# Kernel optimization log

Measured on AMD Instinct MI355X. Metric: run time of the kernel, lower is better.

Reference implementation:

```python
import jax, jax.numpy as jnp
import numpy as np

NUM_HEADS = 16


def setup_inputs() -> dict:
    key = jax.random.key(0)
    ks = jax.random.split(key, 4)
    B, S, H = 2, 2048, 1024
    hidden_states = jax.random.normal(ks[0], (B, S, H), dtype=jnp.float32)
    attention_mask = jnp.zeros((B, 1, 1, S), dtype=jnp.float32)
    scale = 1.0 / np.sqrt(H)
    Wq = jax.random.normal(ks[1], (H, H), dtype=jnp.float32) * scale
    Wk = jax.random.normal(ks[2], (H, H), dtype=jnp.float32) * scale
    Wv = jax.random.normal(ks[3], (H, H), dtype=jnp.float32) * scale
    bq = jnp.zeros((H,), dtype=jnp.float32)
    bk = jnp.zeros((H,), dtype=jnp.float32)
    bv = jnp.zeros((H,), dtype=jnp.float32)
    return {"hidden_states": hidden_states, "attention_mask": attention_mask,
            "Wq": Wq, "bq": bq, "Wk": Wk, "bk": bk, "Wv": Wv, "bv": bv}


def _split_heads(x, B, S):
    # [B, S, H] -> [B, h, S, d]
    return x.reshape(B, S, NUM_HEADS, -1).transpose(0, 2, 1, 3)


def reference(hidden_states, attention_mask, Wq, bq, Wk, bk, Wv, bv):
    B, S, H = hidden_states.shape
    d = H // NUM_HEADS
    q = _split_heads(hidden_states @ Wq + bq, B, S)  # [B,h,S,d]
    k = _split_heads(hidden_states @ Wk + bk, B, S)
    v = _split_heads(hidden_states @ Wv + bv, B, S)

    scores = jnp.einsum('bhqd,bhkd->bhqk', q, k) / jnp.sqrt(jnp.float32(d))
    # causal mask: -inf strictly above diagonal, plus additive pad mask
    i = jnp.arange(S)[:, None]
    j = jnp.arange(S)[None, :]
    causal = jnp.where(j > i, -jnp.inf, 0.0).astype(scores.dtype)  # [S,S]
    scores = scores + attention_mask + causal[None, None, :, :]

    probs = jax.nn.softmax(scores, axis=-1)  # dropout prob = 0.0 -> identity
    context = jnp.einsum('bhqk,bhkd->bhqd', probs, v)  # [B,h,S,d]
    return context.transpose(0, 2, 1, 3).reshape(B, S, H)
```

## Files before the change

kernel.cpp:

```cpp
#include <hip/hip_runtime.h>

typedef __attribute__((ext_vector_type(4)))  float f32x4;
typedef __attribute__((ext_vector_type(16))) float f32x16;
typedef __attribute__((ext_vector_type(8)))  short bf16x8;

typedef __attribute__((address_space(1))) const void gvoid;
typedef __attribute__((address_space(3))) void lvoid;

__device__ __forceinline__ void gl_lds16(const void* g, void* l) {
  __builtin_amdgcn_global_load_lds((gvoid*)g, (lvoid*)l, 16, 0, 0);
}

__device__ __forceinline__ ushort f2bf(float f) {
  union { float f; unsigned u; } v; v.f = f;
  unsigned u = v.u;
  return (ushort)((u + 0x7fffu + ((u >> 16) & 1u)) >> 16);
}

__device__ __forceinline__ uint cvt_pk_bf16(float lo, float hi) {
  uint r;
  asm("v_cvt_pk_bf16_f32 %0, %1, %2" : "=v"(r) : "v"(lo), "v"(hi));
  return r;
}
__device__ __forceinline__ void plswap(uint& x, uint& y) {
  asm volatile("v_permlane32_swap_b32 %0, %1" : "+v"(x), "+v"(y));
}

__global__ __launch_bounds__(256) void cvt_x(const float* __restrict__ x,
                                             ushort* __restrict__ o) {
  int idx = blockIdx.x * 256 + threadIdx.x;
  float4 v = reinterpret_cast<const float4*>(x)[idx];
  ushort4 r;
  r.x = f2bf(v.x); r.y = f2bf(v.y); r.z = f2bf(v.z); r.w = f2bf(v.w);
  reinterpret_cast<ushort4*>(o)[idx] = r;
}

__global__ __launch_bounds__(256) void wtrans(const float* __restrict__ Wq,
                                              const float* __restrict__ Wk,
                                              const float* __restrict__ Wv,
                                              ushort* __restrict__ WT) {
  __shared__ ushort tile[64 * 65];
  int bx = blockIdx.x;
  int w = bx >> 8;
  int rem = bx & 255;
  int k0 = (rem >> 4) << 6;
  int n0 = (rem & 15) << 6;
  const float* W = (w == 0) ? Wq : (w == 1) ? Wk : Wv;
  int tid = threadIdx.x;
#pragma unroll
  for (int it = 0; it < 16; ++it) {
    int idx = tid + it * 256;
    int r = idx >> 6, c = idx & 63;
    tile[r * 65 + c] = f2bf(W[(k0 + r) * 1024 + n0 + c]);
  }
  __syncthreads();
#pragma unroll
  for (int it = 0; it < 16; ++it) {
    int idx = tid + it * 256;
    int r = idx >> 6, c = idx & 63;
    WT[w * 1048576 + (n0 + r) * 1024 + k0 + c] = tile[c * 65 + r];
  }
}

__global__ __launch_bounds__(256) void qkv_gemm(
    const ushort* __restrict__ Xb, const ushort* __restrict__ WT,
    const float* __restrict__ bq, const float* __restrict__ bk,
    const float* __restrict__ bv, ushort* __restrict__ Qb,
    ushort* __restrict__ Kb, ushort* __restrict__ VT) {
  __shared__ ushort smem[128 * 136];
  ushort* Xs = smem;
  ushort* Ws = smem + 8192;
  int tid = threadIdx.x;
  int wave = tid >> 6, lane = tid & 63, g = lane >> 4, lr = lane & 15;
  int wr = wave >> 1, wc = wave & 1;
  int m0 = blockIdx.x << 7;
  int n0g = blockIdx.y << 7;
  f32x4 acc[4][4];
#pragma unroll
  for (int i = 0; i < 4; ++i)
#pragma unroll
    for (int j = 0; j < 4; ++j) { acc[i][j][0] = 0.f; acc[i][j][1] = 0.f; acc[i][j][2] = 0.f; acc[i][j][3] = 0.f; }

  int lrow = lane >> 3, lcol = (lane & 7) * 8;
  for (int k0 = 0; k0 < 1024; k0 += 64) {
    __syncthreads();
#pragma unroll
    for (int c = 0; c < 4; ++c) {
      int cw = wave * 4 + c;
      int row = cw * 8 + lrow;
      gl_lds16(Xb + (size_t)(m0 + row) * 1024 + k0 + lcol, Xs + cw * 512);
      gl_lds16(WT + (size_t)(n0g + row) * 1024 + k0 + lcol, Ws + cw * 512);
    }
    __syncthreads();
#pragma unroll
    for (int ks = 0; ks < 2; ++ks) {
      bf16x8 a[4], b[4];
#pragma unroll
      for (int mi = 0; mi < 4; ++mi)
        a[mi] = *reinterpret_cast<const bf16x8*>(&Xs[(wr * 64 + mi * 16 + lr) * 64 + ks * 32 + g * 8]);
#pragma unroll
      for (int ni = 0; ni < 4; ++ni)
        b[ni] = *reinterpret_cast<const bf16x8*>(&Ws[(wc * 64 + ni * 16 + lr) * 64 + ks * 32 + g * 8]);
      __builtin_amdgcn_s_setprio(1);
#pragma unroll
      for (int mi = 0; mi < 4; ++mi)
#pragma unroll
        for (int ni = 0; ni < 4; ++ni)
          acc[mi][ni] = __builtin_amdgcn_mfma_f32_16x16x32_bf16(a[mi], b[ni], acc[mi][ni], 0, 0, 0);
      __builtin_amdgcn_s_setprio(0);
    }
  }
  __syncthreads();

  int which = n0g >> 10;
  const float* bias = (which == 0) ? bq : (which == 1) ? bk : bv;
  int nloc0 = (n0g & 1023);
  if (which == 2) {
#pragma unroll
    for (int ni = 0; ni < 4; ++ni) {
      int row = wc * 64 + ni * 16 + lr;
      float bb = bias[nloc0 + row];
#pragma unroll
      for (int mi = 0; mi < 4; ++mi) {
        int m = wr * 64 + mi * 16 + g * 4;
        ushort4 v4;
        v4.x = f2bf(acc[mi][ni][0] + bb);
        v4.y = f2bf(acc[mi][ni][1] + bb);
        v4.z = f2bf(acc[mi][ni][2] + bb);
        v4.w = f2bf(acc[mi][ni][3] + bb);
        *reinterpret_cast<ushort4*>(&smem[row * 136 + m]) = v4;
      }
    }
    __syncthreads();
    int b_ = m0 >> 11, s0 = m0 & 2047;
#pragma unroll
    for (int it = 0; it < 8; ++it) {
      int c = tid + it * 256;
      int row = c >> 4, mc = (c & 15) * 8;
      uint4 vv = *reinterpret_cast<const uint4*>(&smem[row * 136 + mc]);
      int n = nloc0 + row;
      int hh = n >> 6, dd = n & 63;
      *reinterpret_cast<uint4*>(&VT[((size_t)(b_ * 16 + hh) * 64 + dd) * 2048 + s0 + mc]) = vv;
    }
  } else {
#pragma unroll
    for (int ni = 0; ni < 4; ++ni) {
      int n = wc * 64 + ni * 16 + lr;
      float bb = bias[nloc0 + n];
#pragma unroll
      for (int mi = 0; mi < 4; ++mi) {
#pragma unroll
        for (int r = 0; r < 4; ++r)
          smem[(wr * 64 + mi * 16 + g * 4 + r) * 136 + n] = f2bf(acc[mi][ni][r] + bb);
      }
    }
    __syncthreads();
    ushort* ob = (which == 0) ? Qb : Kb;
#pragma unroll
    for (int it = 0; it < 8; ++it) {
      int c = tid + it * 256;
      int row = c >> 4, nc = (c & 15) * 8;
      uint4 vv = *reinterpret_cast<const uint4*>(&smem[row * 136 + nc]);
      int m = m0 + row;
      int b_ = m >> 11, s = m & 2047;
      int n = nloc0 + nc;
      int hh = n >> 6, dd = n & 63;
      *reinterpret_cast<uint4*>(&ob[((size_t)(b_ * 16 + hh) * 2048 + s) * 64 + dd]) = vv;
    }
  }
}

__global__ __launch_bounds__(256) void attn(const ushort* __restrict__ Qb,
                                            const ushort* __restrict__ Kb,
                                            const ushort* __restrict__ VT,
                                            const float* __restrict__ mask,
                                            float* __restrict__ out) {
  __shared__ char smem[34816];
  ushort* Ks = (ushort*)smem;
  ushort* Vs = (ushort*)(smem + 8192);
  float*  Ms = (float*)(smem + 16384);
  int tid = threadIdx.x;
  int wave = tid >> 6, lane = tid & 63;
  int hi = lane >> 5, l31 = lane & 31;
  int pi = blockIdx.x & 15, bh = blockIdx.x >> 4;
  int b_ = bh >> 4, h = bh & 15;
  const ushort* Qh = Qb + (size_t)bh * 2048 * 64;
  const ushort* Kh = Kb + (size_t)bh * 2048 * 64;
  const ushort* VTh = VT + (size_t)bh * 64 * 2048;

  int tile = (wave < 2) ? pi : (31 - pi);
  int q0w = tile * 64 + (wave & 1) * 32;
  int tmax = 31 - pi;

  bf16x8 aq[4];
#pragma unroll
  for (int ds = 0; ds < 4; ++ds)
    aq[ds] = *reinterpret_cast<const bf16x8*>(Qh + (q0w + l31) * 64 + ds * 16 + hi * 8);

  f32x16 Od0, Od1;
#pragma unroll
  for (int j = 0; j < 16; ++j) { Od0[j] = 0.f; Od1[j] = 0.f; }
  float mrun = -__builtin_inff(), lrun = 0.f;

  for (int t = 0; t <= tmax; ++t) {
    int kv0 = t << 6;
    __syncthreads();
#pragma unroll
    for (int c = 0; c < 2; ++c) {
      int ch = tid + (c << 8);
      int row = ch >> 3, e0 = (ch & 7) * 8, bc = (ch & 7) << 4;
      int sw = bc ^ ((row & 7) << 4);
      uint4 kvv = *reinterpret_cast<const uint4*>(Kh + (size_t)(kv0 + row) * 64 + e0);
      *reinterpret_cast<uint4*>((char*)Ks + row * 128 + sw) = kvv;
      uint4 vvv = *reinterpret_cast<const uint4*>(VTh + (size_t)row * 2048 + kv0 + e0);
      *reinterpret_cast<uint4*>((char*)Vs + row * 128 + sw) = vvv;
    }
    if (tid < 64) Ms[tid] = mask[b_ * 2048 + kv0 + tid];
    __syncthreads();

#pragma unroll
    for (int sub = 0; sub < 2; ++sub) {
      int kvb = kv0 + sub * 32;
      if (kvb > q0w) continue;
      bool dg = (kvb == q0w);

      f32x16 s;
#pragma unroll
      for (int j = 0; j < 16; ++j) s[j] = 0.f;
      __builtin_amdgcn_s_setprio(1);
#pragma unroll
      for (int ds = 0; ds < 4; ++ds) {
        int krow = sub * 32 + l31;
        bf16x8 kf = *reinterpret_cast<const bf16x8*>(
            (char*)Ks + krow * 128 + ((ds * 32 + hi * 16) ^ ((krow & 7) << 4)));
        s = __builtin_amdgcn_mfma_f32_32x32x16_bf16(kf, aq[ds], s, 0, 0, 0);
      }
      __builtin_amdgcn_s_setprio(0);

#pragma unroll
      for (int jj = 0; jj < 4; ++jj) {
        float4 mv4 = *reinterpret_cast<const float4*>(Ms + sub * 32 + jj * 8 + 4 * hi);
        const float* mvp = (const float*)&mv4;
#pragma unroll
        for (int r = 0; r < 4; ++r) {
          int j = jj * 4 + r;
          float sv = s[j] * 0.125f + mvp[r];
          if (dg) {
            int kvg = kvb + jj * 8 + 4 * hi + r;
            sv = (kvg > q0w + l31) ? -__builtin_inff() : sv;
          }
          s[j] = sv;
        }
      }

      float tmx = s[0];
#pragma unroll
      for (int j = 1; j < 16; ++j) tmx = fmaxf(tmx, s[j]);
      tmx = fmaxf(tmx, __shfl_xor(tmx, 32));
      bool defer = __all(tmx - mrun <= 8.0f);
      float al = 1.0f;
      if (!defer) {
        float nm = fmaxf(mrun, tmx);
        al = __expf(mrun - nm);
        mrun = nm;
      }
      float rs = 0.f;
#pragma unroll
      for (int j = 0; j < 16; ++j) {
        float p = __expf(s[j] - mrun);
        s[j] = p;
        rs += p;
      }
      rs += __shfl_xor(rs, 32);
      lrun = lrun * al + rs;
      if (!defer) {
#pragma unroll
        for (int j = 0; j < 16; ++j) { Od0[j] *= al; Od1[j] *= al; }
      }

      uint x0 = cvt_pk_bf16(s[0], s[1]),   y0 = cvt_pk_bf16(s[4], s[5]);
      uint x1 = cvt_pk_bf16(s[2], s[3]),   y1 = cvt_pk_bf16(s[6], s[7]);
      plswap(x0, y0); plswap(x1, y1);
      uint x2 = cvt_pk_bf16(s[8], s[9]),   y2 = cvt_pk_bf16(s[12], s[13]);
      uint x3 = cvt_pk_bf16(s[10], s[11]), y3 = cvt_pk_bf16(s[14], s[15]);
      plswap(x2, y2); plswap(x3, y3);
      union U { uint w[4]; bf16x8 v; };
      U pa0, pa1;
      pa0.w[0] = x0; pa0.w[1] = x1; pa0.w[2] = y0; pa0.w[3] = y1;
      pa1.w[0] = x2; pa1.w[1] = x3; pa1.w[2] = y2; pa1.w[3] = y3;

      __builtin_amdgcn_s_setprio(1);
#pragma unroll
      for (int ks = 0; ks < 2; ++ks) {
        bf16x8 pf = ks ? pa1.v : pa0.v;
        int bc = sub * 64 + ks * 32 + hi * 16;
        int r0 = l31, r1 = 32 + l31;
        bf16x8 v0 = *reinterpret_cast<const bf16x8*>((char*)Vs + r0 * 128 + (bc ^ ((r0 & 7) << 4)));
        Od0 = __builtin_amdgcn_mfma_f32_32x32x16_bf16(v0, pf, Od0, 0, 0, 0);
        bf16x8 v1 = *reinterpret_cast<const bf16x8*>((char*)Vs + r1 * 128 + (bc ^ ((r1 & 7) << 4)));
        Od1 = __builtin_amdgcn_mfma_f32_32x32x16_bf16(v1, pf, Od1, 0, 0, 0);
      }
      __builtin_amdgcn_s_setprio(0);
    }
  }

  __syncthreads();
  float rl = 1.0f / lrun;
  float* Ot = (float*)smem + wave * (32 * 68);
#pragma unroll
  for (int jj = 0; jj < 4; ++jj) {
    int d0a = jj * 8 + 4 * hi;
    float4 w0, w1;
    w0.x = Od0[jj * 4 + 0] * rl; w0.y = Od0[jj * 4 + 1] * rl;
    w0.z = Od0[jj * 4 + 2] * rl; w0.w = Od0[jj * 4 + 3] * rl;
    w1.x = Od1[jj * 4 + 0] * rl; w1.y = Od1[jj * 4 + 1] * rl;
    w1.z = Od1[jj * 4 + 2] * rl; w1.w = Od1[jj * 4 + 3] * rl;
    *reinterpret_cast<float4*>(&Ot[l31 * 68 + d0a]) = w0;
    *reinterpret_cast<float4*>(&Ot[l31 * 68 + 32 + d0a]) = w1;
  }
  int qr = lane >> 1, half = lane & 1;
  const float* Orow = &Ot[qr * 68 + half * 32];
  float* og = out + (size_t)(b_ * 2048 + q0w + qr) * 1024 + h * 64 + half * 32;
#pragma unroll
  for (int c2 = 0; c2 < 8; ++c2)
    *reinterpret_cast<float4*>(og + c2 * 4) = *reinterpret_cast<const float4*>(Orow + c2 * 4);
}

extern "C" void kernel_launch(void* const* d_in, const int* in_sizes, int n_in,
                              void* d_out, int out_size, void* d_ws, size_t ws_size,
                              hipStream_t stream) {
  const float* X    = (const float*)d_in[0];
  const float* mask = (const float*)d_in[1];
  const float* Wq   = (const float*)d_in[2];
  const float* bq   = (const float*)d_in[3];
  const float* Wk   = (const float*)d_in[4];
  const float* bk   = (const float*)d_in[5];
  const float* Wv   = (const float*)d_in[6];
  const float* bv   = (const float*)d_in[7];
  float* out = (float*)d_out;

  char* ws = (char*)d_ws;
  ushort* Xb  = (ushort*)ws;
  ushort* WTb = (ushort*)(ws + 8388608);
  ushort* Qb  = (ushort*)(ws + 8388608 + 6291456);
  ushort* Kb  = Qb + 4194304;
  ushort* VT  = Kb + 4194304;

  cvt_x<<<4096, 256, 0, stream>>>(X, Xb);
  wtrans<<<768, 256, 0, stream>>>(Wq, Wk, Wv, WTb);
  qkv_gemm<<<dim3(32, 24), 256, 0, stream>>>(Xb, WTb, bq, bk, bv, Qb, Kb, VT);
  attn<<<512, 256, 0, stream>>>(Qb, Kb, VT, mask, out);
}
```

Measured before the change: 238.8 us.

## Pair causal query tiles per wave with double-buffered async K/V staging

The attention kernel now runs 128-thread blocks in which each wave handles both a low and a high causal query tile. Each K fragment read from LDS is reused for two score MFMAs, and each V fragment for two output MFMAs. K/V tiles are loaded with global_load_lds into double-buffered swizzled LDS, prefetching the next tile during compute. Softmax uses exp2 with the log2e factor folded into the scale and mask, and a looser rescale-deferral threshold. The QKV GEMM gets an XOR-swizzled LDS layout to cut bank conflicts and drops setprio, and the weight transpose is vectorised; the trade-offs are higher register pressure per wave and fewer threads per block.

```diff
diff --git a/kernel.cpp b/kernel.cpp
--- a/kernel.cpp
+++ b/kernel.cpp
@@ -9,6 +9,10 @@
 
 __device__ __forceinline__ void gl_lds16(const void* g, void* l) {
   __builtin_amdgcn_global_load_lds((gvoid*)g, (lvoid*)l, 16, 0, 0);
+}
+
+__device__ __forceinline__ float exp2_fast(float x) {
+  return __builtin_amdgcn_exp2f(x);
 }
 
 __device__ __forceinline__ ushort f2bf(float f) {
@@ -39,26 +43,32 @@
                                               const float* __restrict__ Wk,
                                               const float* __restrict__ Wv,
                                               ushort* __restrict__ WT) {
-  __shared__ ushort tile[64 * 65];
+  __shared__ ushort tile[64 * 68];
   int bx = blockIdx.x;
-  int w = bx >> 8;
-  int rem = bx & 255;
-  int k0 = (rem >> 4) << 6;
-  int n0 = (rem & 15) << 6;
+  int w = bx >> 8, rem = bx & 255;
+  int k0 = (rem >> 4) << 6, n0 = (rem & 15) << 6;
   const float* W = (w == 0) ? Wq : (w == 1) ? Wk : Wv;
   int tid = threadIdx.x;
 #pragma unroll
-  for (int it = 0; it < 16; ++it) {
+  for (int it = 0; it < 4; ++it) {
     int idx = tid + it * 256;
-    int r = idx >> 6, c = idx & 63;
-    tile[r * 65 + c] = f2bf(W[(k0 + r) * 1024 + n0 + c]);
+    int r = idx >> 4, c4 = (idx & 15) * 4;
+    float4 v = *reinterpret_cast<const float4*>(&W[(k0 + r) * 1024 + n0 + c4]);
+    ushort4 u;
+    u.x = f2bf(v.x); u.y = f2bf(v.y); u.z = f2bf(v.z); u.w = f2bf(v.w);
+    *reinterpret_cast<ushort4*>(&tile[r * 68 + c4]) = u;
   }
   __syncthreads();
 #pragma unroll
-  for (int it = 0; it < 16; ++it) {
+  for (int it = 0; it < 4; ++it) {
     int idx = tid + it * 256;
-    int r = idx >> 6, c = idx & 63;
-    WT[w * 1048576 + (n0 + r) * 1024 + k0 + c] = tile[c * 65 + r];
+    int n = idx >> 4, k4 = (idx & 15) * 4;
+    ushort4 o;
+    o.x = tile[(k4 + 0) * 68 + n];
+    o.y = tile[(k4 + 1) * 68 + n];
+    o.z = tile[(k4 + 2) * 68 + n];
+    o.w = tile[(k4 + 3) * 68 + n];
+    *reinterpret_cast<ushort4*>(&WT[w * 1048576 + (size_t)(n0 + n) * 1024 + k0 + k4]) = o;
   }
 }
 
@@ -81,33 +91,34 @@
 #pragma unroll
     for (int j = 0; j < 4; ++j) { acc[i][j][0] = 0.f; acc[i][j][1] = 0.f; acc[i][j][2] = 0.f; acc[i][j][3] = 0.f; }
 
-  int lrow = lane >> 3, lcol = (lane & 7) * 8;
+  int l3 = lane >> 3;
+  int jsw = ((lane & 7) ^ l3) * 8;
+  int swz = lr & 7;
   for (int k0 = 0; k0 < 1024; k0 += 64) {
     __syncthreads();
 #pragma unroll
     for (int c = 0; c < 4; ++c) {
       int cw = wave * 4 + c;
-      int row = cw * 8 + lrow;
-      gl_lds16(Xb + (size_t)(m0 + row) * 1024 + k0 + lcol, Xs + cw * 512);
-      gl_lds16(WT + (size_t)(n0g + row) * 1024 + k0 + lcol, Ws + cw * 512);
+      int row = cw * 8 + l3;
+      gl_lds16(Xb + (size_t)(m0 + row) * 1024 + k0 + jsw, Xs + cw * 512);
+      gl_lds16(WT + (size_t)(n0g + row) * 1024 + k0 + jsw, Ws + cw * 512);
     }
     __syncthreads();
 #pragma unroll
     for (int ks = 0; ks < 2; ++ks) {
       bf16x8 a[4], b[4];
+      int slot = ((ks * 4 + g) ^ swz) * 8;
 #pragma unroll
       for (int mi = 0; mi < 4; ++mi)
-        a[mi] = *reinterpret_cast<const bf16x8*>(&Xs[(wr * 64 + mi * 16 + lr) * 64 + ks * 32 + g * 8]);
+        a[mi] = *reinterpret_cast<const bf16x8*>(&Xs[(wr * 64 + mi * 16 + lr) * 64 + slot]);
 #pragma unroll
       for (int ni = 0; ni < 4; ++ni)
-        b[ni] = *reinterpret_cast<const bf16x8*>(&Ws[(wc * 64 + ni * 16 + lr) * 64 + ks * 32 + g * 8]);
-      __builtin_amdgcn_s_setprio(1);
+        b[ni] = *reinterpret_cast<const bf16x8*>(&Ws[(wc * 64 + ni * 16 + lr) * 64 + slot]);
 #pragma unroll
       for (int mi = 0; mi < 4; ++mi)
 #pragma unroll
         for (int ni = 0; ni < 4; ++ni)
           acc[mi][ni] = __builtin_amdgcn_mfma_f32_16x16x32_bf16(a[mi], b[ni], acc[mi][ni], 0, 0, 0);
-      __builtin_amdgcn_s_setprio(0);
     }
   }
   __syncthreads();
@@ -170,143 +181,66 @@
   }
 }
 
-__global__ __launch_bounds__(256) void attn(const ushort* __restrict__ Qb,
-                                            const ushort* __restrict__ Kb,
-                                            const ushort* __restrict__ VT,
-                                            const float* __restrict__ mask,
-                                            float* __restrict__ out) {
-  __shared__ char smem[34816];
-  ushort* Ks = (ushort*)smem;
-  ushort* Vs = (ushort*)(smem + 8192);
-  float*  Ms = (float*)(smem + 16384);
-  int tid = threadIdx.x;
+__device__ __forceinline__ void softmax_state(f32x16& s, float& mrun, float& lrun,
+                                              f32x16& Od0, f32x16& Od1,
+                                              bf16x8& p0, bf16x8& p1) {
+  float tmx = s[0];
+#pragma unroll
+  for (int j = 1; j < 16; ++j) tmx = fmaxf(tmx, s[j]);
+  tmx = fmaxf(tmx, __shfl_xor(tmx, 32));
+  if (!__all(tmx - mrun <= 11.5f)) {
+    float nm = fmaxf(mrun, tmx);
+    float al = exp2_fast(mrun - nm);
+    mrun = nm;
+    lrun *= al;
+#pragma unroll
+    for (int j = 0; j < 16; ++j) { Od0[j] *= al; Od1[j] *= al; }
+  }
+  float rs = 0.f;
+#pragma unroll
+  for (int j = 0; j < 16; ++j) { float p = exp2_fast(s[j] - mrun); s[j] = p; rs += p; }
+  rs += __shfl_xor(rs, 32);
+  lrun += rs;
+  uint x0 = cvt_pk_bf16(s[0], s[1]),   y0 = cvt_pk_bf16(s[4], s[5]);
+  uint x1 = cvt_pk_bf16(s[2], s[3]),   y1 = cvt_pk_bf16(s[6], s[7]);
+  plswap(x0, y0); plswap(x1, y1);
+  uint x2 = cvt_pk_bf16(s[8], s[9]),   y2 = cvt_pk_bf16(s[12], s[13]);
+  uint x3 = cvt_pk_bf16(s[10], s[11]), y3 = cvt_pk_bf16(s[14], s[15]);
+  plswap(x2, y2); plswap(x3, y3);
+  union U { uint w[4]; bf16x8 v; } u0, u1;
+  u0.w[0] = x0; u0.w[1] = x1; u0.w[2] = y0; u0.w[3] = y1;
+  u1.w[0] = x2; u1.w[1] = x3; u1.w[2] = y2; u1.w[3] = y3;
+  p0 = u0.v; p1 = u1.v;
+}
+
+__device__ __forceinline__ void attn_stage(const ushort* Kh, const ushort* VTh,
+                                           const float* maskp, char* smem,
+                                           int buf, int kv0, int tid, int jsw) {
+  ushort* Ksb = (ushort*)(smem + buf * 16384);
+  ushort* Vsb = Ksb + 4096;
   int wave = tid >> 6, lane = tid & 63;
+  int l3 = lane >> 3;
+#pragma unroll
+  for (int c = 0; c < 4; ++c) {
+    int ch = wave * 4 + c;
+    int row = ch * 8 + l3;
+    gl_lds16(Kh + (size_t)(kv0 + row) * 64 + jsw, Ksb + ch * 512);
+    gl_lds16(VTh + (size_t)row * 2048 + kv0 + jsw, Vsb + ch * 512);
+  }
+  if (tid < 16) {
+    float* Msb = (float*)(smem + 32768 + buf * 256);
+    float4 m4 = *reinterpret_cast<const float4*>(maskp + kv0 + tid * 4);
+    m4.x *= 1.44269504f; m4.y *= 1.44269504f; m4.z *= 1.44269504f; m4.w *= 1.44269504f;
+    *reinterpret_cast<float4*>(Msb + tid * 4) = m4;
+  }
+}
+
+__device__ __forceinline__ void attn_writeout(char* smem, int wave, int lane,
+                                              const f32x16& Od0, const f32x16& Od1,
+                                              float lrun, float* outp, int q0w) {
+  float* Ot = (float*)smem + wave * 2176;
   int hi = lane >> 5, l31 = lane & 31;
-  int pi = blockIdx.x & 15, bh = blockIdx.x >> 4;
-  int b_ = bh >> 4, h = bh & 15;
-  const ushort* Qh = Qb + (size_t)bh * 2048 * 64;
-  const ushort* Kh = Kb + (size_t)bh * 2048 * 64;
-  const ushort* VTh = VT + (size_t)bh * 64 * 2048;
-
-  int tile = (wave < 2) ? pi : (31 - pi);
-  int q0w = tile * 64 + (wave & 1) * 32;
-  int tmax = 31 - pi;
-
-  bf16x8 aq[4];
-#pragma unroll
-  for (int ds = 0; ds < 4; ++ds)
-    aq[ds] = *reinterpret_cast<const bf16x8*>(Qh + (q0w + l31) * 64 + ds * 16 + hi * 8);
-
-  f32x16 Od0, Od1;
-#pragma unroll
-  for (int j = 0; j < 16; ++j) { Od0[j] = 0.f; Od1[j] = 0.f; }
-  float mrun = -__builtin_inff(), lrun = 0.f;
-
-  for (int t = 0; t <= tmax; ++t) {
-    int kv0 = t << 6;
-    __syncthreads();
-#pragma unroll
-    for (int c = 0; c < 2; ++c) {
-      int ch = tid + (c << 8);
-      int row = ch >> 3, e0 = (ch & 7) * 8, bc = (ch & 7) << 4;
-      int sw = bc ^ ((row & 7) << 4);
-      uint4 kvv = *reinterpret_cast<const uint4*>(Kh + (size_t)(kv0 + row) * 64 + e0);
-      *reinterpret_cast<uint4*>((char*)Ks + row * 128 + sw) = kvv;
-      uint4 vvv = *reinterpret_cast<const uint4*>(VTh + (size_t)row * 2048 + kv0 + e0);
-      *reinterpret_cast<uint4*>((char*)Vs + row * 128 + sw) = vvv;
-    }
-    if (tid < 64) Ms[tid] = mask[b_ * 2048 + kv0 + tid];
-    __syncthreads();
-
-#pragma unroll
-    for (int sub = 0; sub < 2; ++sub) {
-      int kvb = kv0 + sub * 32;
-      if (kvb > q0w) continue;
-      bool dg = (kvb == q0w);
-
-      f32x16 s;
-#pragma unroll
-      for (int j = 0; j < 16; ++j) s[j] = 0.f;
-      __builtin_amdgcn_s_setprio(1);
-#pragma unroll
-      for (int ds = 0; ds < 4; ++ds) {
-        int krow = sub * 32 + l31;
-        bf16x8 kf = *reinterpret_cast<const bf16x8*>(
-            (char*)Ks + krow * 128 + ((ds * 32 + hi * 16) ^ ((krow & 7) << 4)));
-        s = __builtin_amdgcn_mfma_f32_32x32x16_bf16(kf, aq[ds], s, 0, 0, 0);
-      }
-      __builtin_amdgcn_s_setprio(0);
-
-#pragma unroll
-      for (int jj = 0; jj < 4; ++jj) {
-        float4 mv4 = *reinterpret_cast<const float4*>(Ms + sub * 32 + jj * 8 + 4 * hi);
-        const float* mvp = (const float*)&mv4;
-#pragma unroll
-        for (int r = 0; r < 4; ++r) {
-          int j = jj * 4 + r;
-          float sv = s[j] * 0.125f + mvp[r];
-          if (dg) {
-            int kvg = kvb + jj * 8 + 4 * hi + r;
-            sv = (kvg > q0w + l31) ? -__builtin_inff() : sv;
-          }
-          s[j] = sv;
-        }
-      }
-
-      float tmx = s[0];
-#pragma unroll
-      for (int j = 1; j < 16; ++j) tmx = fmaxf(tmx, s[j]);
-      tmx = fmaxf(tmx, __shfl_xor(tmx, 32));
-      bool defer = __all(tmx - mrun <= 8.0f);
-      float al = 1.0f;
-      if (!defer) {
-        float nm = fmaxf(mrun, tmx);
-        al = __expf(mrun - nm);
-        mrun = nm;
-      }
-      float rs = 0.f;
-#pragma unroll
-      for (int j = 0; j < 16; ++j) {
-        float p = __expf(s[j] - mrun);
-        s[j] = p;
-        rs += p;
-      }
-      rs += __shfl_xor(rs, 32);
-      lrun = lrun * al + rs;
-      if (!defer) {
-#pragma unroll
-        for (int j = 0; j < 16; ++j) { Od0[j] *= al; Od1[j] *= al; }
-      }
-
-      uint x0 = cvt_pk_bf16(s[0], s[1]),   y0 = cvt_pk_bf16(s[4], s[5]);
-      uint x1 = cvt_pk_bf16(s[2], s[3]),   y1 = cvt_pk_bf16(s[6], s[7]);
-      plswap(x0, y0); plswap(x1, y1);
-      uint x2 = cvt_pk_bf16(s[8], s[9]),   y2 = cvt_pk_bf16(s[12], s[13]);
-      uint x3 = cvt_pk_bf16(s[10], s[11]), y3 = cvt_pk_bf16(s[14], s[15]);
-      plswap(x2, y2); plswap(x3, y3);
-      union U { uint w[4]; bf16x8 v; };
-      U pa0, pa1;
-      pa0.w[0] = x0; pa0.w[1] = x1; pa0.w[2] = y0; pa0.w[3] = y1;
-      pa1.w[0] = x2; pa1.w[1] = x3; pa1.w[2] = y2; pa1.w[3] = y3;
-
-      __builtin_amdgcn_s_setprio(1);
-#pragma unroll
-      for (int ks = 0; ks < 2; ++ks) {
-        bf16x8 pf = ks ? pa1.v : pa0.v;
-        int bc = sub * 64 + ks * 32 + hi * 16;
-        int r0 = l31, r1 = 32 + l31;
-        bf16x8 v0 = *reinterpret_cast<const bf16x8*>((char*)Vs + r0 * 128 + (bc ^ ((r0 & 7) << 4)));
-        Od0 = __builtin_amdgcn_mfma_f32_32x32x16_bf16(v0, pf, Od0, 0, 0, 0);
-        bf16x8 v1 = *reinterpret_cast<const bf16x8*>((char*)Vs + r1 * 128 + (bc ^ ((r1 & 7) << 4)));
-        Od1 = __builtin_amdgcn_mfma_f32_32x32x16_bf16(v1, pf, Od1, 0, 0, 0);
-      }
-      __builtin_amdgcn_s_setprio(0);
-    }
-  }
-
-  __syncthreads();
   float rl = 1.0f / lrun;
-  float* Ot = (float*)smem + wave * (32 * 68);
 #pragma unroll
   for (int jj = 0; jj < 4; ++jj) {
     int d0a = jj * 8 + 4 * hi;
@@ -320,10 +254,153 @@
   }
   int qr = lane >> 1, half = lane & 1;
   const float* Orow = &Ot[qr * 68 + half * 32];
-  float* og = out + (size_t)(b_ * 2048 + q0w + qr) * 1024 + h * 64 + half * 32;
+  float* og = outp + (size_t)(q0w + qr) * 1024 + half * 32;
 #pragma unroll
   for (int c2 = 0; c2 < 8; ++c2)
     *reinterpret_cast<float4*>(og + c2 * 4) = *reinterpret_cast<const float4*>(Orow + c2 * 4);
+}
+
+__global__ __launch_bounds__(128) void attn(const ushort* __restrict__ Qb,
+                                            const ushort* __restrict__ Kb,
+                                            const ushort* __restrict__ VT,
+                                            const float* __restrict__ mask,
+                                            float* __restrict__ out) {
+  __shared__ char smem[33280];
+  const float SCALE = 0.125f * 1.44269504f;
+  int tid = threadIdx.x;
+  int wave = tid >> 6, lane = tid & 63;
+  int hi = lane >> 5, l31 = lane & 31;
+  int jsw = ((lane & 7) ^ (lane >> 3)) * 8;
+  int pi = blockIdx.x & 15, bh = blockIdx.x >> 4;
+  int b_ = bh >> 4, h = bh & 15;
+  const ushort* Qh = Qb + (size_t)bh * 131072;
+  const ushort* Kh = Kb + (size_t)bh * 131072;
+  const ushort* VTh = VT + (size_t)bh * 131072;
+  const float* maskp = mask + b_ * 2048;
+  int qa0 = pi * 64 + wave * 32;
+  int qb0 = (31 - pi) * 64 + wave * 32;
+  int tmax = 31 - pi;
+
+  bf16x8 aqa[4], aqb[4];
+#pragma unroll
+  for (int ds = 0; ds < 4; ++ds) {
+    aqa[ds] = *reinterpret_cast<const bf16x8*>(Qh + (qa0 + l31) * 64 + ds * 16 + hi * 8);
+    aqb[ds] = *reinterpret_cast<const bf16x8*>(Qh + (qb0 + l31) * 64 + ds * 16 + hi * 8);
+  }
+
+  f32x16 OA0, OA1, OB0, OB1;
+#pragma unroll
+  for (int j = 0; j < 16; ++j) { OA0[j] = 0.f; OA1[j] = 0.f; OB0[j] = 0.f; OB1[j] = 0.f; }
+  float mA = -__builtin_inff(), lA = 0.f, mB = -__builtin_inff(), lB = 0.f;
+
+  attn_stage(Kh, VTh, maskp, smem, 0, 0, tid, jsw);
+
+  for (int t = 0; t <= tmax; ++t) {
+    int cur = t & 1;
+    __syncthreads();
+    if (t < tmax) attn_stage(Kh, VTh, maskp, smem, cur ^ 1, (t + 1) << 6, tid, jsw);
+    ushort* Ksb = (ushort*)(smem + cur * 16384);
+    ushort* Vsb = Ksb + 4096;
+    const float* Msb = (const float*)(smem + 32768 + cur * 256);
+    int kv0 = t << 6;
+#pragma unroll
+    for (int sub = 0; sub < 2; ++sub) {
+      int kvb = kv0 + sub * 32;
+      bool actA = (kvb <= qa0), actB = (kvb <= qb0);
+      if (!actB && !actA) continue;
+      bf16x8 kf[4];
+      int krow = sub * 32 + l31;
+      int ksw = krow & 7;
+#pragma unroll
+      for (int ds = 0; ds < 4; ++ds)
+        kf[ds] = *reinterpret_cast<const bf16x8*>(Ksb + krow * 64 + (((ds * 2 + hi) ^ ksw) * 8));
+      f32x16 sB, sA;
+      __builtin_amdgcn_s_setprio(1);
+      if (actB) {
+#pragma unroll
+        for (int j = 0; j < 16; ++j) sB[j] = 0.f;
+#pragma unroll
+        for (int ds = 0; ds < 4; ++ds)
+          sB = __builtin_amdgcn_mfma_f32_32x32x16_bf16(kf[ds], aqb[ds], sB, 0, 0, 0);
+      }
+      if (actA) {
+#pragma unroll
+        for (int j = 0; j < 16; ++j) sA[j] = 0.f;
+#pragma unroll
+        for (int ds = 0; ds < 4; ++ds)
+          sA = __builtin_amdgcn_mfma_f32_32x32x16_bf16(kf[ds], aqa[ds], sA, 0, 0, 0);
+      }
+      __builtin_amdgcn_s_setprio(0);
+
+      float4 mv[4];
+#pragma unroll
+      for (int jj = 0; jj < 4; ++jj)
+        mv[jj] = *reinterpret_cast<const float4*>(Msb + sub * 32 + jj * 8 + 4 * hi);
+
+      bf16x8 pB0, pB1, pA0, pA1;
+      if (actB) {
+        bool dg = (kvb == qb0);
+#pragma unroll
+        for (int jj = 0; jj < 4; ++jj) {
+          const float* mvp = (const float*)&mv[jj];
+#pragma unroll
+          for (int r = 0; r < 4; ++r) {
+            int j = jj * 4 + r;
+            float v = sB[j] * SCALE + mvp[r];
+            if (dg) {
+              int kvg = kvb + jj * 8 + 4 * hi + r;
+              v = (kvg > qb0 + l31) ? -__builtin_inff() : v;
+            }
+            sB[j] = v;
+          }
+        }
+        softmax_state(sB, mB, lB, OB0, OB1, pB0, pB1);
+      }
+      if (actA) {
+        bool dg = (kvb == qa0);
+#pragma unroll
+        for (int jj = 0; jj < 4; ++jj) {
+          const float* mvp = (const float*)&mv[jj];
+#pragma unroll
+          for (int r = 0; r < 4; ++r) {
+            int j = jj * 4 + r;
+            float v = sA[j] * SCALE + mvp[r];
+            if (dg) {
+              int kvg = kvb + jj * 8 + 4 * hi + r;
+              v = (kvg > qa0 + l31) ? -__builtin_inff() : v;
+            }
+            sA[j] = v;
+          }
+        }
+        softmax_state(sA, mA, lA, OA0, OA1, pA0, pA1);
+      }
+
+      __builtin_amdgcn_s_setprio(1);
+#pragma unroll
+      for (int ks = 0; ks < 2; ++ks) {
+#pragma unroll
+        for (int h2 = 0; h2 < 2; ++h2) {
+          int drow = h2 * 32 + l31;
+          bf16x8 vf = *reinterpret_cast<const bf16x8*>(
+              Vsb + drow * 64 + (((sub * 4 + ks * 2 + hi) ^ (drow & 7)) * 8));
+          if (actB) {
+            f32x16& O = h2 ? OB1 : OB0;
+            O = __builtin_amdgcn_mfma_f32_32x32x16_bf16(vf, ks ? pB1 : pB0, O, 0, 0, 0);
+          }
+          if (actA) {
+            f32x16& O = h2 ? OA1 : OA0;
+            O = __builtin_amdgcn_mfma_f32_32x32x16_bf16(vf, ks ? pA1 : pA0, O, 0, 0, 0);
+          }
+        }
+      }
+      __builtin_amdgcn_s_setprio(0);
+    }
+  }
+
+  __syncthreads();
+  float* outp = out + (size_t)b_ * 2048 * 1024 + h * 64;
+  attn_writeout(smem, wave, lane, OA0, OA1, lA, outp, qa0);
+  attn_writeout(smem, wave, lane, OB0, OB1, lB, outp, qb0);
 }
 
 extern "C" void kernel_launch(void* const* d_in, const int* in_sizes, int n_in,
@@ -349,5 +426,5 @@
   cvt_x<<<4096, 256, 0, stream>>>(X, Xb);
   wtrans<<<768, 256, 0, stream>>>(Wq, Wk, Wv, WTb);
   qkv_gemm<<<dim3(32, 24), 256, 0, stream>>>(Xb, WTb, bq, bk, bv, Qb, Kb, VT);
-  attn<<<512, 256, 0, stream>>>(Qb, Kb, VT, mask, out);
-}
+  attn<<<512, 128, 0, stream>>>(Qb, Kb, VT, mask, out);
+}
```

Result: faster. 224.6 us (-6.0%).
